# Optimization experiments

Measured on AMD Instinct MI355X. Metric: run time of the kernel, lower is better.

Reference implementation:

```python
import jax, jax.numpy as jnp
import numpy as np

N, E, D_IN, HID, HEADS = 50000, 800000, 128, 32, 8
NEG_SLOPE = 0.2


def gat_conv(x, src, dst, W_src, W_dst, a_src, a_dst, b, heads, ch, concat):
    n = x.shape[0]
    hs = (x @ W_src).reshape(n, heads, ch)  # source-side features [N,H,C]
    hd = (x @ W_dst).reshape(n, heads, ch)  # dest-side features   [N,H,C]
    alpha_s = jnp.einsum('nhc,hc->nh', hs, a_src)  # [N,H]
    alpha_d = jnp.einsum('nhc,hc->nh', hd, a_dst)  # [N,H]
    e = jax.nn.leaky_relu(alpha_s[src] + alpha_d[dst], NEG_SLOPE)  # [E,H]
    # segment softmax over edges grouped by destination node
    m = jax.ops.segment_max(e, dst, num_segments=n)
    m = jnp.where(jnp.isfinite(m), m, 0.0)
    e = jnp.exp(e - jax.lax.stop_gradient(m)[dst])
    denom = jax.ops.segment_sum(e, dst, num_segments=n)
    alpha = e / (denom[dst] + 1e-16)  # [E,H]
    # weighted scatter-aggregate of source features to destinations
    out = jax.ops.segment_sum(hs[src] * alpha[:, :, None], dst, num_segments=n)  # [N,H,C]
    out = out.reshape(n, heads * ch) if concat else out.mean(axis=1)
    return out + b


def setup_inputs() -> dict:
    key = jax.random.key(0)
    ks = jax.random.split(key, 12)
    glorot = lambda k, shape: jax.random.normal(k, shape, jnp.float32) * np.sqrt(2.0 / (shape[0] + shape[-1]))
    x = jax.random.normal(ks[0], (N, D_IN), jnp.float32)
    edge_index = jax.random.randint(ks[1], (2, E), 0, N, jnp.int64)
    return {
        'x': x,
        'edge_index': edge_index,
        'W1_src': glorot(ks[2], (D_IN, HEADS * HID)),
        'W1_dst': glorot(ks[3], (D_IN, HEADS * HID)),
        'a1_src': glorot(ks[4], (HEADS, HID)),
        'a1_dst': glorot(ks[5], (HEADS, HID)),
        'b1': jnp.zeros((HEADS * HID,), jnp.float32),
        'W2_src': glorot(ks[6], (HEADS * HID, HID)),
        'W2_dst': glorot(ks[7], (HEADS * HID, HID)),
        'a2_src': glorot(ks[8], (1, HID)),
        'a2_dst': glorot(ks[9], (1, HID)),
        'b2': jnp.zeros((HID,), jnp.float32),
    }


def reference(x, edge_index, W1_src, W1_dst, a1_src, a1_dst, b1,
              W2_src, W2_dst, a2_src, a2_dst, b2):
    src, dst = edge_index[0], edge_index[1]
    h = gat_conv(x, src, dst, W1_src, W1_dst, a1_src, a1_dst, b1, HEADS, HID, True)
    h = jax.nn.relu(h)
    out = gat_conv(h, src, dst, W2_src, W2_dst, a2_src, a2_dst, b2, 1, HID, True)
    return out
```

## Files before the change

### kernel.cpp

```cpp
#include <hip/hip_runtime.h>
#include <hip/hip_bf16.h>

#define NEG_SLOPE 0.2f

typedef unsigned int uint;
typedef unsigned short ushort;
typedef __attribute__((ext_vector_type(8))) short short8;
typedef __attribute__((ext_vector_type(4))) float floatx4;

static __device__ __forceinline__ ushort f2bf(float f) {
    uint u = __float_as_uint(f);
    uint r = (u + 0x7fffu + ((u >> 16) & 1u)) >> 16;
    return (ushort)r;
}
static __device__ __forceinline__ float bf2f(uint s) {
    return __uint_as_float(s << 16);
}

__global__ __launch_bounds__(256) void histprep_kernel(
    const int* __restrict__ dst, int* __restrict__ deg, int E, int HB,
    const float* __restrict__ W1_src, const float* __restrict__ a1_src,
    const float* __restrict__ W1_dst, const float* __restrict__ a1_dst,
    const float* __restrict__ W2_src, const float* __restrict__ a2_src,
    const float* __restrict__ W2_dst, const float* __restrict__ a2_dst,
    ushort* __restrict__ W1e, ushort* __restrict__ W2e) {
    if (blockIdx.x < (uint)HB) {
        int i = blockIdx.x * blockDim.x + threadIdx.x;
        int e0 = i * 2;
        if (e0 + 1 < E) {
            int2 d2 = ((const int2*)dst)[i];
            atomicAdd(&deg[d2.x], 1);
            atomicAdd(&deg[d2.y], 1);
        } else if (e0 < E) {
            atomicAdd(&deg[dst[e0]], 1);
        }
        return;
    }
    int i = (blockIdx.x - HB) * blockDim.x + threadIdx.x;
    if (i < 32768) {
        int nc = i & 255, k = i >> 8;
        W1e[nc * 128 + k] = f2bf(W1_src[k * 256 + nc]);
    } else if (i < 34816) {
        int j = i - 32768;
        int h = (j >> 7) & 7, k = j & 127;
        bool is_ws = j < 1024;
        const float* W = is_ws ? W1_src : W1_dst;
        const float* a = is_ws ? a1_src : a1_dst;
        float s = 0.f;
#pragma unroll
        for (int c = 0; c < 32; ++c)
            s += W[k * 256 + h * 32 + c] * a[h * 32 + c];
        W1e[((is_ws ? 256 : 264) + h) * 128 + k] = f2bf(s);
    } else if (i < 34816 + 8192) {
        int j = i - 34816;
        int c = j & 31, k = j >> 5;
        W2e[c * 256 + k] = f2bf(W2_src[k * 32 + c]);
    } else if (i < 34816 + 8192 + 512) {
        int j = i - 34816 - 8192;
        int k = j & 255;
        bool is_ws = j < 256;
        const float* W = is_ws ? W2_src : W2_dst;
        const float* a = is_ws ? a2_src : a2_dst;
        float s = 0.f;
#pragma unroll
        for (int c = 0; c < 32; ++c) s += W[k * 32 + c] * a[c];
        W2e[(is_ws ? 32 : 33) * 256 + k] = f2bf(s);
    } else if (i < 34816 + 8192 + 512 + 3584) {
        int j = i - 34816 - 8192 - 512;
        W2e[34 * 256 + j] = 0;
    }
}

__global__ __launch_bounds__(256) void scanrs_kernel(
    const int* __restrict__ deg, int* __restrict__ rs,
    int* __restrict__ cursor, int* __restrict__ agg,
    int* __restrict__ flag, int n, int E) {
    __shared__ int sh[256];
    int tid = threadIdx.x;
    int c = blockIdx.x;
    int i = c * 256 + tid;
    int d = (i < n) ? deg[i] : 0;
    sh[tid] = d;
    __syncthreads();
    for (int off = 1; off < 256; off <<= 1) {
        int t = (tid >= off) ? sh[tid - off] : 0;
        __syncthreads();
        sh[tid] += t;
        __syncthreads();
    }
    int incl = sh[tid];
    if (tid == 255) {
        agg[c] = incl;
        __threadfence();
        __hip_atomic_store(&flag[c], 1, __ATOMIC_RELEASE,
                           __HIP_MEMORY_SCOPE_AGENT);
    }
    int vt = 0;
    if (tid < c) {
        while (__hip_atomic_load(&flag[tid], __ATOMIC_ACQUIRE,
                                 __HIP_MEMORY_SCOPE_AGENT) == 0) {}
        vt = agg[tid];
    }
    __syncthreads();
    sh[tid] = vt;
    __syncthreads();
    for (int off = 128; off > 0; off >>= 1) {
        if (tid < off) sh[tid] += sh[tid + off];
        __syncthreads();
    }
    int boff = sh[0];
    if (i < n) {
        int v = incl - d + boff;
        rs[i] = v;
        cursor[i] = v;
    }
    if (c == 0 && tid == 0) rs[n] = E;
}

__global__ __launch_bounds__(256) void fill_kernel(
    const int* __restrict__ src, const int* __restrict__ dst,
    int* __restrict__ cursor, int* __restrict__ csr_src, int E) {
    int i = blockIdx.x * blockDim.x + threadIdx.x;
    int e0 = i * 2;
    if (e0 + 1 < E) {
        int2 d2 = ((const int2*)dst)[i];
        int2 s2 = ((const int2*)src)[i];
        int p0 = atomicAdd(&cursor[d2.x], 1);
        int p1 = atomicAdd(&cursor[d2.y], 1);
        csr_src[p0] = s2.x;
        csr_src[p1] = s2.y;
    } else if (e0 < E) {
        int pos = atomicAdd(&cursor[dst[e0]], 1);
        csr_src[pos] = src[e0];
    }
}

__global__ __launch_bounds__(256) void gemm1_mfma(
    const float* __restrict__ x, const ushort* __restrict__ W1e,
    ushort* __restrict__ hs1b, float* __restrict__ as1,
    float* __restrict__ ad1, int n) {
    __shared__ ushort buf[128 * 128];
    int mblk = blockIdx.x >> 1, nhalf = blockIdx.x & 1;
    int m0 = mblk * 128;
    int tid = threadIdx.x;
#pragma unroll
    for (int i = 0; i < 8; ++i) {
        int id = tid + i * 256;
        int m = id >> 4, c = id & 15;
        int gm = m0 + m;
        uint4 pk = {0, 0, 0, 0};
        if (gm < n) {
            const float4* xp = (const float4*)(x + (size_t)gm * 128 + c * 8);
            float4 v0 = xp[0], v1 = xp[1];
            pk.x = (uint)f2bf(v0.x) | ((uint)f2bf(v0.y) << 16);
            pk.y = (uint)f2bf(v0.z) | ((uint)f2bf(v0.w) << 16);
            pk.z = (uint)f2bf(v1.x) | ((uint)f2bf(v1.y) << 16);
            pk.w = (uint)f2bf(v1.z) | ((uint)f2bf(v1.w) << 16);
        }
        *(uint4*)(buf + m * 128 + ((c ^ (m & 15)) * 8)) = pk;
    }
    __syncthreads();
    int wid = tid >> 6, lane = tid & 63;
    int q = lane >> 4, l16 = lane & 15;
    int wm = (wid >> 1) * 64;
    int wn = (wid & 1) * 64;
    int gn0 = nhalf * 128 + wn;
    bool do_e = (nhalf == 0) && ((wid & 1) == 0);
    floatx4 z = {0.f, 0.f, 0.f, 0.f};
    floatx4 acc[4][4];
    floatx4 acc_e[4] = {z, z, z, z};
#pragma unroll
    for (int mt = 0; mt < 4; ++mt)
#pragma unroll
        for (int nt = 0; nt < 4; ++nt) acc[mt][nt] = z;
#pragma unroll
    for (int s = 0; s < 4; ++s) {
        short8 af[4], bf[4];
#pragma unroll
        for (int mt = 0; mt < 4; ++mt) {
            int row = wm + mt * 16 + l16;
            int c = s * 4 + q;
            af[mt] = *(const short8*)(buf + row * 128 + ((c ^ (row & 15)) * 8));
        }
#pragma unroll
        for (int nt = 0; nt < 4; ++nt) {
            int col = gn0 + nt * 16 + l16;
            bf[nt] = *(const short8*)(W1e + col * 128 + s * 32 + q * 8);
        }
#pragma unroll
        for (int mt = 0; mt < 4; ++mt)
#pragma unroll
            for (int nt = 0; nt < 4; ++nt)
                acc[mt][nt] = __builtin_amdgcn_mfma_f32_16x16x32_bf16(
                    af[mt], bf[nt], acc[mt][nt], 0, 0, 0);
        if (do_e) {
            short8 bfe = *(const short8*)(W1e + (256 + l16) * 128 + s * 32 + q * 8);
#pragma unroll
            for (int mt = 0; mt < 4; ++mt)
                acc_e[mt] = __builtin_amdgcn_mfma_f32_16x16x32_bf16(
                    af[mt], bfe, acc_e[mt], 0, 0, 0);
        }
    }
    __syncthreads();
#pragma unroll
    for (int mt = 0; mt < 4; ++mt)
#pragma unroll
        for (int nt = 0; nt < 4; ++nt) {
            floatx4 a = acc[mt][nt];
            int colL = wn + nt * 16 + l16;
#pragma unroll
            for (int r = 0; r < 4; ++r) {
                int rowL = wm + mt * 16 + q * 4 + r;
                buf[rowL * 128 + (((colL >> 3) ^ (rowL & 15)) * 8) + (colL & 7)]
                    = f2bf(a[r]);
            }
        }
    if (do_e) {
#pragma unroll
        for (int mt = 0; mt < 4; ++mt) {
            floatx4 ae = acc_e[mt];
#pragma unroll
            for (int r = 0; r < 4; ++r) {
                int gm = m0 + wm + mt * 16 + q * 4 + r;
                if (gm < n) {
                    if (l16 < 8) as1[(size_t)gm * 8 + l16] = ae[r];
                    else         ad1[(size_t)gm * 8 + l16 - 8] = ae[r];
                }
            }
        }
    }
    __syncthreads();
#pragma unroll
    for (int i = 0; i < 8; ++i) {
        int id = tid + i * 256;
        int m = id >> 4, c8 = id & 15;
        int gm = m0 + m;
        if (gm < n) {
            uint4 v = *(uint4*)(buf + m * 128 + ((c8 ^ (m & 15)) * 8));
            *(uint4*)(hs1b + (size_t)gm * 256 + nhalf * 128 + c8 * 8) = v;
        }
    }
}

__global__ __launch_bounds__(256) void gather1(
    const int* __restrict__ csr_src, const int* __restrict__ rs,
    const ushort* __restrict__ hs1b, const float* __restrict__ as1,
    const float* __restrict__ ad1, const float* __restrict__ b1,
    ushort* __restrict__ h1b, int n) {
    int gid = blockIdx.x * blockDim.x + threadIdx.x;
    int node = gid >> 6;
    int lane = threadIdx.x & 63;
    if (node >= n) return;
    int j = lane >> 5, l = lane & 31;
    int h = l >> 2;
    float ad_v = ad1[node * 8 + h];
    int start = rs[node], cnt = rs[node + 1] - start;
    float acc0 = 0.f, acc1 = 0.f, acc2 = 0.f, acc3 = 0.f;
    float acc4 = 0.f, acc5 = 0.f, acc6 = 0.f, acc7 = 0.f;
    float dacc = 0.f;
    int i = j;
    for (; i + 2 < cnt; i += 4) {
        int sA = csr_src[start + i];
        int sB = csr_src[start + i + 2];
        float tA = as1[sA * 8 + h] + ad_v;
        float tB = as1[sB * 8 + h] + ad_v;
        uint4 vA = *(const uint4*)(hs1b + (size_t)sA * 256 + l * 8);
        uint4 vB = *(const uint4*)(hs1b + (size_t)sB * 256 + l * 8);
        tA = (tA >= 0.f) ? tA : NEG_SLOPE * tA;
        tB = (tB >= 0.f) ? tB : NEG_SLOPE * tB;
        float wA = __expf(tA);
        float wB = __expf(tB);
        acc0 += bf2f(vA.x & 0xffffu) * wA + bf2f(vB.x & 0xffffu) * wB;
        acc1 += bf2f(vA.x >> 16) * wA + bf2f(vB.x >> 16) * wB;
        acc2 += bf2f(vA.y & 0xffffu) * wA + bf2f(vB.y & 0xffffu) * wB;
        acc3 += bf2f(vA.y >> 16) * wA + bf2f(vB.y >> 16) * wB;
        acc4 += bf2f(vA.z & 0xffffu) * wA + bf2f(vB.z & 0xffffu) * wB;
        acc5 += bf2f(vA.z >> 16) * wA + bf2f(vB.z >> 16) * wB;
        acc6 += bf2f(vA.w & 0xffffu) * wA + bf2f(vB.w & 0xffffu) * wB;
        acc7 += bf2f(vA.w >> 16) * wA + bf2f(vB.w >> 16) * wB;
        dacc += wA + wB;
    }
    for (; i < cnt; i += 2) {
        int s = csr_src[start + i];
        float t = as1[s * 8 + h] + ad_v;
        uint4 v = *(const uint4*)(hs1b + (size_t)s * 256 + l * 8);
        t = (t >= 0.f) ? t : NEG_SLOPE * t;
        float w = __expf(t);
        acc0 += bf2f(v.x & 0xffffu) * w;
        acc1 += bf2f(v.x >> 16) * w;
        acc2 += bf2f(v.y & 0xffffu) * w;
        acc3 += bf2f(v.y >> 16) * w;
        acc4 += bf2f(v.z & 0xffffu) * w;
        acc5 += bf2f(v.z >> 16) * w;
        acc6 += bf2f(v.w & 0xffffu) * w;
        acc7 += bf2f(v.w >> 16) * w;
        dacc += w;
    }
    acc0 += __shfl_xor(acc0, 32, 64);
    acc1 += __shfl_xor(acc1, 32, 64);
    acc2 += __shfl_xor(acc2, 32, 64);
    acc3 += __shfl_xor(acc3, 32, 64);
    acc4 += __shfl_xor(acc4, 32, 64);
    acc5 += __shfl_xor(acc5, 32, 64);
    acc6 += __shfl_xor(acc6, 32, 64);
    acc7 += __shfl_xor(acc7, 32, 64);
    dacc += __shfl_xor(dacc, 32, 64);
    if (j == 0) {
        float inv = 1.f / (dacc + 1e-16f);
        float4 b0 = ((const float4*)b1)[l * 2];
        float4 b4 = ((const float4*)b1)[l * 2 + 1];
        float o0 = fmaxf(fmaf(acc0, inv, b0.x), 0.f);
        float o1 = fmaxf(fmaf(acc1, inv, b0.y), 0.f);
        float o2 = fmaxf(fmaf(acc2, inv, b0.z), 0.f);
        float o3 = fmaxf(fmaf(acc3, inv, b0.w), 0.f);
        float o4 = fmaxf(fmaf(acc4, inv, b4.x), 0.f);
        float o5 = fmaxf(fmaf(acc5, inv, b4.y), 0.f);
        float o6 = fmaxf(fmaf(acc6, inv, b4.z), 0.f);
        float o7 = fmaxf(fmaf(acc7, inv, b4.w), 0.f);
        uint4 pk;
        pk.x = (uint)f2bf(o0) | ((uint)f2bf(o1) << 16);
        pk.y = (uint)f2bf(o2) | ((uint)f2bf(o3) << 16);
        pk.z = (uint)f2bf(o4) | ((uint)f2bf(o5) << 16);
        pk.w = (uint)f2bf(o6) | ((uint)f2bf(o7) << 16);
        *(uint4*)(h1b + (size_t)node * 256 + l * 8) = pk;
    }
}

__global__ __launch_bounds__(256) void gemm2_mfma(
    const ushort* __restrict__ h1b, const ushort* __restrict__ W2e,
    ushort* __restrict__ hs2b, float* __restrict__ as2,
    float* __restrict__ ad2, int n) {
    __shared__ ushort At[64 * 256];
    __shared__ ushort Out[64 * 32];
    int m0 = blockIdx.x * 64;
    int tid = threadIdx.x;
#pragma unroll
    for (int i = 0; i < 8; ++i) {
        int id = tid + i * 256;
        int m = id >> 5, c = id & 31;
        int gm = m0 + m;
        uint4 v = {0, 0, 0, 0};
        if (gm < n) v = *(const uint4*)(h1b + (size_t)gm * 256 + c * 8);
        *(uint4*)(At + m * 256 + ((c ^ (m & 15)) * 8)) = v;
    }
    __syncthreads();
    int wid = tid >> 6, lane = tid & 63;
    int q = lane >> 4, l16 = lane & 15;
    int wm = wid * 16;
    floatx4 z = {0.f, 0.f, 0.f, 0.f};
    floatx4 acc[2] = {z, z};
    floatx4 acc_e = z;
#pragma unroll
    for (int s = 0; s < 8; ++s) {
        int row = wm + l16;
        int c = s * 4 + q;
        short8 af = *(const short8*)(At + row * 256 + ((c ^ (row & 15)) * 8));
        short8 bf0 = *(const short8*)(W2e + l16 * 256 + s * 32 + q * 8);
        short8 bf1 = *(const short8*)(W2e + (16 + l16) * 256 + s * 32 + q * 8);
        short8 bfe = *(const short8*)(W2e + (32 + l16) * 256 + s * 32 + q * 8);
        acc[0] = __builtin_amdgcn_mfma_f32_16x16x32_bf16(af, bf0, acc[0], 0, 0, 0);
        acc[1] = __builtin_amdgcn_mfma_f32_16x16x32_bf16(af, bf1, acc[1], 0, 0, 0);
        acc_e  = __builtin_amdgcn_mfma_f32_16x16x32_bf16(af, bfe, acc_e, 0, 0, 0);
    }
#pragma unroll
    for (int nt = 0; nt < 2; ++nt) {
        floatx4 a = acc[nt];
        int colL = nt * 16 + l16;
#pragma unroll
        for (int r = 0; r < 4; ++r) {
            int rowL = wm + q * 4 + r;
            Out[rowL * 32 + (((colL >> 3) ^ (rowL & 3)) * 8) + (colL & 7)]
                = f2bf(a[r]);
        }
    }
#pragma unroll
    for (int r = 0; r < 4; ++r) {
        int gm = m0 + wm + q * 4 + r;
        if (gm < n) {
            if (l16 == 0) as2[gm] = acc_e[r];
            else if (l16 == 1) ad2[gm] = acc_e[r];
        }
    }
    __syncthreads();
    {
        int id = tid;
        int c4 = id & 3, m = id >> 2;
        int gm = m0 + m;
        if (gm < n)
            *(uint4*)(hs2b + (size_t)gm * 32 + c4 * 8) =
                *(uint4*)(Out + m * 32 + ((c4 ^ (m & 3)) * 8));
    }
}

__global__ __launch_bounds__(256) void gather2(
    const int* __restrict__ csr_src, const int* __restrict__ rs,
    const ushort* __restrict__ hs2b, const float* __restrict__ as2,
    const float* __restrict__ ad2, const float* __restrict__ b2,
    float* __restrict__ out, int n) {
    int gid = blockIdx.x * blockDim.x + threadIdx.x;
    int node = gid >> 6;
    int lane = threadIdx.x & 63;
    if (node >= n) return;
    int g = lane >> 3, l = lane & 7;
    float ad_v = ad2[node];
    int start = rs[node], cnt = rs[node + 1] - start;
    float a0 = 0.f, a1 = 0.f, a2 = 0.f, a3 = 0.f, dacc = 0.f;
    for (int i = g; i < cnt; i += 8) {
        int s = csr_src[start + i];
        float t = as2[s] + ad_v;
        t = (t >= 0.f) ? t : NEG_SLOPE * t;
        float w = __expf(t);
        uint2 v = *(const uint2*)(hs2b + (size_t)s * 32 + l * 4);
        a0 += bf2f(v.x & 0xffffu) * w;
        a1 += bf2f(v.x >> 16) * w;
        a2 += bf2f(v.y & 0xffffu) * w;
        a3 += bf2f(v.y >> 16) * w;
        dacc += w;
    }
#pragma unroll
    for (int m = 8; m <= 32; m <<= 1) {
        a0 += __shfl_xor(a0, m, 64);
        a1 += __shfl_xor(a1, m, 64);
        a2 += __shfl_xor(a2, m, 64);
        a3 += __shfl_xor(a3, m, 64);
        dacc += __shfl_xor(dacc, m, 64);
    }
    if (g == 0) {
        float inv = 1.f / (dacc + 1e-16f);
        float4 bv = ((const float4*)b2)[l];
        float4 o;
        o.x = fmaf(a0, inv, bv.x);
        o.y = fmaf(a1, inv, bv.y);
        o.z = fmaf(a2, inv, bv.z);
        o.w = fmaf(a3, inv, bv.w);
        *(float4*)(out + (size_t)node * 32 + l * 4) = o;
    }
}

extern "C" void kernel_launch(void* const* d_in, const int* in_sizes, int n_in,
                              void* d_out, int out_size, void* d_ws, size_t ws_size,
                              hipStream_t stream) {
    const float* x      = (const float*)d_in[0];
    const int*   eidx   = (const int*)d_in[1];
    const float* W1_src = (const float*)d_in[2];
    const float* W1_dst = (const float*)d_in[3];
    const float* a1_src = (const float*)d_in[4];
    const float* a1_dst = (const float*)d_in[5];
    const float* b1     = (const float*)d_in[6];
    const float* W2_src = (const float*)d_in[7];
    const float* W2_dst = (const float*)d_in[8];
    const float* a2_src = (const float*)d_in[9];
    const float* a2_dst = (const float*)d_in[10];
    const float* b2     = (const float*)d_in[11];

    const int n = in_sizes[0] / 128;
    const int E = in_sizes[1] / 2;
    const int* srcp = eidx;
    const int* dstp = eidx + E;
    const int nb = (n + 255) / 256;

    char* ws = (char*)d_ws;
    size_t o = 0;
    auto alloc = [&](size_t bytes) {
        void* p = ws + o;
        o += (bytes + 255) & ~(size_t)255;
        return p;
    };
    ushort* W1e  = (ushort*)alloc(272 * 128 * 2);
    ushort* W2e  = (ushort*)alloc(48 * 256 * 2);
    ushort* hs1b = (ushort*)alloc((size_t)n * 256 * 2);
    ushort* h1b  = (ushort*)alloc((size_t)n * 256 * 2);
    ushort* hs2b = (ushort*)alloc((size_t)n * 32 * 2);
    float* as1 = (float*)alloc((size_t)n * 8 * 4);
    float* ad1 = (float*)alloc((size_t)n * 8 * 4);
    float* as2 = (float*)alloc((size_t)n * 4);
    float* ad2 = (float*)alloc((size_t)n * 4);
    int* csrmeta = (int*)alloc(((size_t)n + 512) * 4);
    int* deg  = csrmeta;
    int* agg  = csrmeta + n;
    int* flag = csrmeta + n + 256;
    int* rs      = (int*)alloc(((size_t)n + 1) * 4);
    int* cursor  = (int*)alloc((size_t)n * 4);
    int* csr_src = (int*)alloc((size_t)E * 4);

    hipMemsetAsync(csrmeta, 0, ((size_t)n + 512) * sizeof(int), stream);

    const int HB = (E / 2 + 255) / 256;
    const int PB = (34816 + 8192 + 512 + 3584 + 255) / 256;
    histprep_kernel<<<HB + PB, 256, 0, stream>>>(
        dstp, deg, E, HB, W1_src, a1_src, W1_dst, a1_dst,
        W2_src, a2_src, W2_dst, a2_dst, W1e, W2e);
    scanrs_kernel<<<nb, 256, 0, stream>>>(deg, rs, cursor, agg, flag, n, E);
    fill_kernel<<<(E / 2 + 255) / 256, 256, 0, stream>>>(srcp, dstp, cursor,
                                                         csr_src, E);

    gemm1_mfma<<<((n + 127) / 128) * 2, 256, 0, stream>>>(
        x, W1e, hs1b, as1, ad1, n);
    gather1<<<(n + 3) / 4, 256, 0, stream>>>(
        csr_src, rs, hs1b, as1, ad1, b1, h1b, n);

    gemm2_mfma<<<(n + 63) / 64, 256, 0, stream>>>(
        h1b, W2e, hs2b, as2, ad2, n);
    gather2<<<(n + 3) / 4, 256, 0, stream>>>(
        csr_src, rs, hs2b, as2, ad2, b2, (float*)d_out, n);
}
```

Baseline: 321.5 us.

## Fuse CSR fill into gemm1 launch as extra blocks to overlap work

Merges the CSR fill kernel and the layer-1 MFMA GEMM into one launch, with the first GB blocks doing the GEMM and the remaining blocks doing the atomic scatter fill. The two tasks are independent, so this removes a launch boundary and lets the latency-bound atomic fill run alongside the compute-bound GEMM. In exchange, the fill blocks now reserve the GEMM's 32KB shared memory, which can lower occupancy. The fill also drops from two edges per thread to one.

```diff
diff --git a/kernel.cpp b/kernel.cpp
--- a/kernel.cpp
+++ b/kernel.cpp
@@ -117,29 +117,22 @@
     if (c == 0 && tid == 0) rs[n] = E;
 }
 
-__global__ __launch_bounds__(256) void fill_kernel(
+__global__ __launch_bounds__(256) void fillgemm1_kernel(
+    const float* __restrict__ x, const ushort* __restrict__ W1e,
+    ushort* __restrict__ hs1b, float* __restrict__ as1,
+    float* __restrict__ ad1, int n, int GB,
     const int* __restrict__ src, const int* __restrict__ dst,
     int* __restrict__ cursor, int* __restrict__ csr_src, int E) {
-    int i = blockIdx.x * blockDim.x + threadIdx.x;
-    int e0 = i * 2;
-    if (e0 + 1 < E) {
-        int2 d2 = ((const int2*)dst)[i];
-        int2 s2 = ((const int2*)src)[i];
-        int p0 = atomicAdd(&cursor[d2.x], 1);
-        int p1 = atomicAdd(&cursor[d2.y], 1);
-        csr_src[p0] = s2.x;
-        csr_src[p1] = s2.y;
-    } else if (e0 < E) {
-        int pos = atomicAdd(&cursor[dst[e0]], 1);
-        csr_src[pos] = src[e0];
-    }
-}
-
-__global__ __launch_bounds__(256) void gemm1_mfma(
-    const float* __restrict__ x, const ushort* __restrict__ W1e,
-    ushort* __restrict__ hs1b, float* __restrict__ as1,
-    float* __restrict__ ad1, int n) {
     __shared__ ushort buf[128 * 128];
+    if (blockIdx.x >= (uint)GB) {
+        int e = (blockIdx.x - GB) * blockDim.x + threadIdx.x;
+        if (e < E) {
+            int d = dst[e];
+            int pos = atomicAdd(&cursor[d], 1);
+            csr_src[pos] = src[e];
+        }
+        return;
+    }
     int mblk = blockIdx.x >> 1, nhalf = blockIdx.x & 1;
     int m0 = mblk * 128;
     int tid = threadIdx.x;
@@ -491,11 +484,12 @@
         dstp, deg, E, HB, W1_src, a1_src, W1_dst, a1_dst,
         W2_src, a2_src, W2_dst, a2_dst, W1e, W2e);
     scanrs_kernel<<<nb, 256, 0, stream>>>(deg, rs, cursor, agg, flag, n, E);
-    fill_kernel<<<(E / 2 + 255) / 256, 256, 0, stream>>>(srcp, dstp, cursor,
-                                                         csr_src, E);
-
-    gemm1_mfma<<<((n + 127) / 128) * 2, 256, 0, stream>>>(
-        x, W1e, hs1b, as1, ad1, n);
+
+    const int GB = ((n + 127) / 128) * 2;
+    const int FB = (E + 255) / 256;
+    fillgemm1_kernel<<<GB + FB, 256, 0, stream>>>(
+        x, W1e, hs1b, as1, ad1, n, GB, srcp, dstp, cursor, csr_src, E);
+
     gather1<<<(n + 3) / 4, 256, 0, stream>>>(
         csr_src, rs, hs1b, as1, ad1, b1, h1b, n);
 
```

New measurement: 315.1 us. 2.0% less time.
